# Kernel tuning notes

Hardware: AMD Instinct MI355X
Metric: run time of the kernel (lower is better)

## Reference

```python
import jax, jax.numpy as jnp
import numpy as np

T, B = 32, 64
D_IN = 512      # input_size == embedding dim
H = 512         # hidden_size
V = 32000       # n_vocab
F_FEAT = 768    # feature_size
NH = 8          # num_heads
HD = H // NH    # head_dim


def setup_inputs() -> dict:
    key = jax.random.key(0)
    ks = jax.random.split(key, 16)
    s = 0.02
    inp = {
        'y': jax.random.randint(ks[0], (T, B), 0, V),
        'ctx': jax.random.normal(ks[1], (1, B, F_FEAT), jnp.float32),
        'emb_W': jax.random.normal(ks[2], (V, D_IN), jnp.float32) * s,
        # GRUCell dec0: gates ordered (r, z, n) as in torch
        'W_ih': jax.random.normal(ks[3], (3 * H, D_IN), jnp.float32) * s,
        'b_ih': jnp.zeros((3 * H,), jnp.float32),
        'W_hh': jax.random.normal(ks[4], (3 * H, H), jnp.float32) * s,
        'b_hh': jnp.zeros((3 * H,), jnp.float32),
        # FF att: feature_size -> hidden, tanh
        'W_att': jax.random.normal(ks[5], (H, F_FEAT), jnp.float32) * s,
        'b_att': jnp.zeros((H,), jnp.float32),
        # MultiHeadSelfAttention projections (hidden -> hidden)
        'Wq': jax.random.normal(ks[6], (H, H), jnp.float32) * s,
        'bq': jnp.zeros((H,), jnp.float32),
        'Wk': jax.random.normal(ks[7], (H, H), jnp.float32) * s,
        'bk': jnp.zeros((H,), jnp.float32),
        'Wv': jax.random.normal(ks[8], (H, H), jnp.float32) * s,
        'bv': jnp.zeros((H,), jnp.float32),
        'Wfc': jax.random.normal(ks[9], (H, H), jnp.float32) * s,
        'bfc': jnp.zeros((H,), jnp.float32),
        # FF hid2out: hidden -> input, tanh, bias_zero
        'W_h2o': jax.random.normal(ks[10], (D_IN, H), jnp.float32) * s,
        'b_h2o': jnp.zeros((D_IN,), jnp.float32),
        # FF out2prob: input -> vocab, linear
        'W_out': jax.random.normal(ks[11], (V, D_IN), jnp.float32) * s,
        'b_out': jnp.zeros((V,), jnp.float32),
    }
    return inp


def reference(y, ctx, emb_W, W_ih, b_ih, W_hh, b_hh, W_att, b_att,
              Wq, bq, Wk, bk, Wv, bv, Wfc, bfc, W_h2o, b_h2o, W_out, b_out):
    y_emb = emb_W[y]                                   # [T, B, D_IN]
    # ct is constant across decode steps: tanh FF over pooled image feature
    ct = jnp.tanh(ctx[0] @ W_att.T + b_att)            # [B, H]
    h0 = jnp.zeros((y.shape[1], H), y_emb.dtype)       # dec_init 'zero'

    def step(h, y_t):
        # torch GRUCell (gate order r, z, n)
        gi = y_t @ W_ih.T + b_ih                       # [B, 3H]
        gh = h @ W_hh.T + b_hh                         # [B, 3H]
        gi_r, gi_z, gi_n = jnp.split(gi, 3, axis=-1)
        gh_r, gh_z, gh_n = jnp.split(gh, 3, axis=-1)
        r = jax.nn.sigmoid(gi_r + gh_r)
        z = jax.nn.sigmoid(gi_z + gh_z)
        n = jnp.tanh(gi_n + r * gh_n)
        h1 = (1.0 - z) * n + z * h                     # [B, H]

        x = h1 * ct                                    # [B, H]
        # MultiHeadSelfAttention on a single vector, heads act as sequence
        q = (x @ Wq.T + bq).reshape(-1, NH, HD)        # [B, NH, HD]
        k = (x @ Wk.T + bk).reshape(-1, NH, HD)
        v = (x @ Wv.T + bv).reshape(-1, NH, HD)
        scores = jnp.einsum('bhd,bgd->bhg', q, k) / HD  # note: /head_dim (not sqrt)
        attw = jax.nn.softmax(scores, axis=-1)
        att_out = jnp.einsum('bhg,bgd->bhd', attw, v).reshape(-1, H)
        h2 = att_out @ Wfc.T + bfc                     # [B, H] (fc_out, vocab_size==H)

        logit = jnp.tanh(h2 @ W_h2o.T + b_h2o)         # [B, D_IN]
        prob = jax.nn.softmax(logit @ W_out.T + b_out, axis=-1)  # [B, V]
        return h1, prob                                # f_next returns h1 as next state

    _, probs = jax.lax.scan(step, h0, y_emb)           # [T, B, V]
    return probs
```

## Files before the change

### kernel.cpp

```cpp
#include <hip/hip_runtime.h>
#include <hip/hip_bf16.h>
#include <math.h>

typedef __bf16 bf16_t;
typedef __bf16 bf16x8 __attribute__((ext_vector_type(8)));
typedef __bf16 bf16x4 __attribute__((ext_vector_type(4)));
typedef float  f32x4  __attribute__((ext_vector_type(4)));

#define T_STEPS 32
#define BATCH   64
#define DIN     512
#define HID     512
#define VOCAB   32000
#define FFEAT   768
#define ROWS    2048
#define G3      1536
#define NBLK_A  32

#define EPI_F32  0
#define EPI_BF16 1
#define EPI_TANH 2

#define GLOAD16(gp, lp) __builtin_amdgcn_global_load_lds( \
    (const __attribute__((address_space(1))) void*)(gp),  \
    (__attribute__((address_space(3))) void*)(lp), 16, 0, 0)

#define PHASEK(BUF, MH, KS, STAGE_STMT, GATE_STMT)                            \
  {                                                                           \
    bf16x8 af_[4], bf_[4];                                                    \
    _Pragma("unroll")                                                         \
    for (int m2 = 0; m2 < 4; ++m2) {                                          \
      const int row = wm * 64 + m2 * 16 + la;                                 \
      const int sl = ((KS) * 4 + lg) ^ (row & 7);                             \
      af_[m2] =                                                               \
          *(const bf16x8*)&lds[((BUF)*4 + (MH)) * 8192 + row * 64 + sl * 8];  \
    }                                                                         \
    _Pragma("unroll")                                                         \
    for (int nj = 0; nj < 4; ++nj) {                                          \
      const int row = wn * 32 + (nj & 1) * 16 + la;                           \
      const int sl = ((KS) * 4 + lg) ^ (row & 7);                             \
      bf_[nj] =                                                               \
          *(const bf16x8*)&lds[((BUF)*4 + 2 + (nj >> 1)) * 8192 + row * 64 + sl * 8];\
    }                                                                         \
    STAGE_STMT;                                                               \
    GATE_STMT;                                                                \
    __builtin_amdgcn_s_barrier();                                             \
    __builtin_amdgcn_s_setprio(1);                                            \
    _Pragma("unroll")                                                         \
    for (int m2 = 0; m2 < 4; ++m2)                                            \
      _Pragma("unroll")                                                       \
      for (int nj = 0; nj < 4; ++nj)                                          \
        acc[(MH)*4 + m2][nj] =                                                \
            __builtin_amdgcn_mfma_f32_16x16x32_bf16(                          \
                af_[m2], bf_[nj], acc[(MH)*4 + m2][nj], 0, 0, 0);             \
    __builtin_amdgcn_s_setprio(0);                                            \
    __builtin_amdgcn_s_barrier();                                             \
  }

template<int KD>
__global__ __launch_bounds__(512, 2) void gemm_v(
    const bf16_t* __restrict__ A, const bf16_t* __restrict__ B,
    const float* __restrict__ bias, bf16_t* __restrict__ ecache,
    float* __restrict__ partial, int M, int N, int NB)
{
  __shared__ bf16_t lds[2 * 4 * 8192];
  __shared__ float psum[256][4];
  const int tid = threadIdx.x;
  const int lane = tid & 63, wv = tid >> 6;
  const int wm = wv >> 2, wn = wv & 3;
  const int la = lane & 15, lg = lane >> 4;

  const int lin = blockIdx.x;
  const int mt = M >> 8;
  const int cpx = (NB * mt) >> 3;
  const int wg = (lin & 7) * cpx + (lin >> 3);
  const int bn = wg / mt, bm = wg - bn * mt;

  auto stageA = [&](int buf, int h, int kt) {
    const size_t base = (size_t)(bm * 256 + h * 128) * KD + (size_t)kt * 64;
#pragma unroll
    for (int q = 0; q < 2; ++q) {
      const int L = q * 512 + tid;
      const int row = L >> 3, sl = L & 7;
      const int c = sl ^ (row & 7);
      GLOAD16(A + base + (size_t)row * KD + c * 8,
              &lds[(buf * 4 + h) * 8192 + L * 8]);
    }
  };
  auto stageB = [&](int buf, int h, int kt) {
    const size_t base = (size_t)(bn * 256 + h * 128) * KD + (size_t)kt * 64;
#pragma unroll
    for (int q = 0; q < 2; ++q) {
      const int L = q * 512 + tid;
      const int row = L >> 3, sl = L & 7;
      const int c = sl ^ (row & 7);
      GLOAD16(B + base + (size_t)row * KD + c * 8,
              &lds[(buf * 4 + 2 + h) * 8192 + L * 8]);
    }
  };

  f32x4 acc[8][4] = {};
  constexpr int NITER = KD >> 7;

  stageA(0, 0, 0); stageA(0, 1, 0); stageB(0, 0, 0); stageB(0, 1, 0);
  stageA(1, 0, 1);
  asm volatile("s_waitcnt vmcnt(2)" ::: "memory");
  __builtin_amdgcn_s_barrier();

#pragma unroll
  for (int it = 0; it < NITER; ++it) {
    const int t0 = 2 * it;
    const bool lastI = (it == NITER - 1);
    PHASEK(0, 0, 0, { stageA(1, 1, t0 + 1); stageB(1, 0, t0 + 1); }, ;)
    PHASEK(0, 0, 1, { stageB(1, 1, t0 + 1); }, ;)
    PHASEK(0, 1, 0, { if (!lastI) stageA(0, 0, t0 + 2); }, ;)
    PHASEK(0, 1, 1, { },
           { if (lastI) { asm volatile("s_waitcnt vmcnt(0)" ::: "memory"); }
             else       { asm volatile("s_waitcnt vmcnt(2)" ::: "memory"); } })
    PHASEK(1, 0, 0, { if (!lastI) { stageA(0, 1, t0 + 2); stageB(0, 0, t0 + 2); } }, ;)
    PHASEK(1, 0, 1, { if (!lastI) stageB(0, 1, t0 + 2); }, ;)
    PHASEK(1, 1, 0, { if (!lastI) stageA(1, 0, t0 + 3); }, ;)
    PHASEK(1, 1, 1, { },
           { if (!lastI) { asm volatile("s_waitcnt vmcnt(2)" ::: "memory"); } })
  }

  float bv[4];
#pragma unroll
  for (int nj = 0; nj < 4; ++nj) {
    const int col = bn * 256 + (nj >> 1) * 128 + wn * 32 + (nj & 1) * 16 + la;
    bv[nj] = bias[col];
  }
  const int odd = la & 1;
#pragma unroll
  for (int mi = 0; mi < 8; ++mi) {
#pragma unroll
    for (int rr = 0; rr < 4; ++rr) {
      const int rowl = (mi >> 2) * 128 + wm * 64 + (mi & 3) * 16 + lg * 4 + rr;
      const int row = bm * 256 + rowl;
      float vsum = 0.f;
#pragma unroll
      for (int nj = 0; nj < 4; ++nj) {
        const float e = expf(acc[mi][nj][rr] + bv[nj]);
        vsum += e;
        const unsigned int mine =
            (unsigned int)__builtin_bit_cast(unsigned short, (bf16_t)e);
        const unsigned int other = (unsigned int)__shfl_xor((int)mine, 1);
        if (!odd) {
          const int col = bn * 256 + (nj >> 1) * 128 + wn * 32 + (nj & 1) * 16 + la;
          *(unsigned int*)&ecache[(size_t)row * N + col] = mine | (other << 16);
        }
      }
      vsum += __shfl_xor(vsum, 1);
      vsum += __shfl_xor(vsum, 2);
      vsum += __shfl_xor(vsum, 4);
      vsum += __shfl_xor(vsum, 8);
      if (la == 0) psum[rowl][wn] = vsum;
    }
  }
  __syncthreads();
  if (tid < 256) {
    partial[(size_t)(bm * 256 + tid) * NB + bn] =
        psum[tid][0] + psum[tid][1] + psum[tid][2] + psum[tid][3];
  }
}

template<int EPI, int KD>
__global__ __launch_bounds__(256) void gemm_lds(
    const bf16_t* __restrict__ A, const bf16_t* __restrict__ B,
    const float* __restrict__ bias, void* __restrict__ out, int M, int N)
{
  __shared__ bf16_t As[3][128 * 32];
  __shared__ bf16_t Bs[3][128 * 32];

  const int lane = threadIdx.x & 63;
  const int wv   = threadIdx.x >> 6;
  const int wm = wv >> 1, wn = wv & 1;
  const int bn = blockIdx.x, bm = blockIdx.y;
  const int la = lane & 15, lg = lane >> 4;
  const int tid = threadIdx.x;

  auto stage = [&](int buf, int k0) {
#pragma unroll
    for (int q = 0; q < 2; ++q) {
      const int idx = q * 256 + tid;
      const int row = idx >> 2, c = idx & 3;
      const int gch = c ^ ((row >> 1) & 3);
      GLOAD16(A + (size_t)(bm * 128 + row) * KD + k0 + gch * 8, &As[buf][idx * 8]);
      GLOAD16(B + (size_t)(bn * 128 + row) * KD + k0 + gch * 8, &Bs[buf][idx * 8]);
    }
  };
  const int rdch = (lg ^ ((la >> 1) & 3)) * 8;

  f32x4 acc[4][4] = {};
  constexpr int NT = KD >> 5;
  stage(0, 0);
  stage(1, 32);
  for (int kt = 0; kt < NT; ++kt) {
    if (kt + 1 < NT) {
      asm volatile("s_waitcnt vmcnt(4)" ::: "memory");
    } else {
      asm volatile("s_waitcnt vmcnt(0)" ::: "memory");
    }
    __builtin_amdgcn_s_barrier();
    __builtin_amdgcn_sched_barrier(0);
    if (kt + 2 < NT) stage((kt + 2) % 3, (kt + 2) * 32);
    const bf16_t* Ab = As[kt % 3];
    const bf16_t* Bb = Bs[kt % 3];
    bf16x8 a[4], b[4];
#pragma unroll
    for (int i = 0; i < 4; ++i)
      a[i] = *(const bf16x8*)(Ab + (wm * 64 + i * 16 + la) * 32 + rdch);
#pragma unroll
    for (int j = 0; j < 4; ++j)
      b[j] = *(const bf16x8*)(Bb + (wn * 64 + j * 16 + la) * 32 + rdch);
    __builtin_amdgcn_s_setprio(1);
#pragma unroll
    for (int i = 0; i < 4; ++i)
#pragma unroll
      for (int j = 0; j < 4; ++j)
        acc[i][j] = __builtin_amdgcn_mfma_f32_16x16x32_bf16(a[i], b[j], acc[i][j], 0, 0, 0);
    __builtin_amdgcn_s_setprio(0);
  }

  const int m0 = bm * 128 + wm * 64;
  const int n0 = bn * 128 + wn * 64;
  float bv4[4];
#pragma unroll
  for (int j = 0; j < 4; ++j) bv4[j] = bias[n0 + j * 16 + la];
#pragma unroll
  for (int i = 0; i < 4; ++i) {
#pragma unroll
    for (int r = 0; r < 4; ++r) {
      const int row = m0 + i * 16 + lg * 4 + r;
#pragma unroll
      for (int j = 0; j < 4; ++j) {
        const int col = n0 + j * 16 + la;
        float v = acc[i][j][r] + bv4[j];
        if constexpr (EPI == EPI_F32) {
          ((float*)out)[(size_t)row * N + col] = v;
        } else if constexpr (EPI == EPI_BF16) {
          ((bf16_t*)out)[(size_t)row * N + col] = (bf16_t)v;
        } else {
          ((bf16_t*)out)[(size_t)row * N + col] = (bf16_t)tanhf(v);
        }
      }
    }
  }
}

__global__ __launch_bounds__(256) void phaseA_k(
    const bf16_t* __restrict__ Wg, const float* __restrict__ bhh,
    const float* __restrict__ gi, const float* __restrict__ ct,
    unsigned int* __restrict__ hbuf, bf16_t* __restrict__ Xall,
    int* __restrict__ flags, const float* __restrict__ Wout_f32,
    bf16_t* __restrict__ WoutB)
{
  __shared__ bf16_t Wl[48 * 520];
  __shared__ float bl[48];
  const int tid = threadIdx.x, blk = blockIdx.x;

  if (blk >= NBLK_A) {
    const int NCB = gridDim.x - NBLK_A;
    const int n4 = VOCAB * DIN / 4;
    for (int i = (blk - NBLK_A) * 256 + tid; i < n4; i += NCB * 256) {
      float4 v = ((const float4*)Wout_f32)[i];
      bf16x4 o = {(bf16_t)v.x, (bf16_t)v.y, (bf16_t)v.z, (bf16_t)v.w};
      *(bf16x4*)(WoutB + (size_t)i * 4) = o;
    }
    return;
  }

  for (int i = tid; i < 48 * 64; i += 256) {
    const int rw = i >> 6, ch = (i & 63) << 3;
    *(bf16x8*)(Wl + rw * 520 + ch) = *(const bf16x8*)(Wg + (size_t)(blk * 48 + rw) * 512 + ch);
  }
  if (tid < 48) bl[tid] = bhh[blk * 48 + tid];
  __syncthreads();

  const int lane = tid & 63, wv = tid >> 6;
  const int la = lane & 15, lg = lane >> 4;
  const int jcol = blk * 16 + la;
  const int rowA = wv * 16 + la;

  const float blr = bl[la], blz = bl[16 + la], bln = bl[32 + la];
  float hprev[4], ctv[4];
#pragma unroll
  for (int r = 0; r < 4; ++r) {
    hprev[r] = 0.f;
    ctv[r] = ct[(size_t)(wv * 16 + lg * 4 + r) * HID + jcol];
  }

  for (int t = 0; t < T_STEPS; ++t) {
    const float* girow = gi + (size_t)t * BATCH * G3 + (size_t)blk * 48;
    float gv[12];
#pragma unroll
    for (int r = 0; r < 4; ++r) {
      const float* gp = girow + (size_t)(wv * 16 + lg * 4 + r) * G3;
      gv[r * 3 + 0] = gp[la];
      gv[r * 3 + 1] = gp[16 + la];
      gv[r * 3 + 2] = gp[32 + la];
    }
    if (t > 0) {
      if (lane < 32) {
        while (__hip_atomic_load(&flags[(lane * 4 + wv) * 16], __ATOMIC_RELAXED,
                                 __HIP_MEMORY_SCOPE_AGENT) < t) { }
      }
      asm volatile("" ::: "memory");
    }
    const unsigned long long* hb =
        (const unsigned long long*)(hbuf + (size_t)(t & 1) * 16384);
    bf16x8 af[16];
#pragma unroll
    for (int q = 0; q < 16; ++q) {
      union { unsigned long long u[2]; bf16x8 v; } c;
      const size_t bidx = (size_t)(2 * q + (lg >> 1)) * 256 + rowA * 4 + (lg & 1) * 2;
      c.u[0] = __hip_atomic_load(hb + bidx,     __ATOMIC_RELAXED, __HIP_MEMORY_SCOPE_AGENT);
      c.u[1] = __hip_atomic_load(hb + bidx + 1, __ATOMIC_RELAXED, __HIP_MEMORY_SCOPE_AGENT);
      af[q] = c.v;
    }
    f32x4 acc0 = {}, acc1 = {}, acc2 = {};
#pragma unroll
    for (int q = 0; q < 16; ++q) {
      const bf16_t* wp = Wl + q * 32 + lg * 8;
      bf16x8 b0 = *(const bf16x8*)(wp + (0 * 16 + la) * 520);
      bf16x8 b1 = *(const bf16x8*)(wp + (1 * 16 + la) * 520);
      bf16x8 b2 = *(const bf16x8*)(wp + (2 * 16 + la) * 520);
      acc0 = __builtin_amdgcn_mfma_f32_16x16x32_bf16(af[q], b0, acc0, 0, 0, 0);
      acc1 = __builtin_amdgcn_mfma_f32_16x16x32_bf16(af[q], b1, acc1, 0, 0, 0);
      acc2 = __builtin_amdgcn_mfma_f32_16x16x32_bf16(af[q], b2, acc2, 0, 0, 0);
    }
    float h1v[4];
#pragma unroll
    for (int r = 0; r < 4; ++r) {
      const float ghr = acc0[r] + blr;
      const float ghz = acc1[r] + blz;
      const float ghn = acc2[r] + bln;
      const float rr = 1.f / (1.f + expf(-(gv[r * 3 + 0] + ghr)));
      const float zz = 1.f / (1.f + expf(-(gv[r * 3 + 1] + ghz)));
      const float nn = tanhf(gv[r * 3 + 2] + rr * ghn);
      h1v[r] = (1.f - zz) * nn + zz * hprev[r];
      hprev[r] = h1v[r];
    }
    unsigned int* hn = hbuf + (size_t)((t + 1) & 1) * 16384 + blk * 512;
#pragma unroll
    for (int r = 0; r < 4; ++r) {
      const int row = wv * 16 + lg * 4 + r;
      const unsigned int mine =
          (unsigned int)__builtin_bit_cast(unsigned short, (bf16_t)h1v[r]);
      const unsigned int other = (unsigned int)__shfl_xor((int)mine, 1);
      if ((la & 1) == 0) {
        __hip_atomic_store(hn + row * 8 + (la >> 1), mine | (other << 16),
                           __ATOMIC_RELAXED, __HIP_MEMORY_SCOPE_AGENT);
      }
    }
    asm volatile("s_waitcnt vmcnt(0)" ::: "memory");
    if (lane == 0) {
      __hip_atomic_store(&flags[(blk * 4 + wv) * 16], t + 1, __ATOMIC_RELAXED,
                         __HIP_MEMORY_SCOPE_AGENT);
    }
#pragma unroll
    for (int r = 0; r < 4; ++r) {
      const int row = wv * 16 + lg * 4 + r;
      Xall[((size_t)t * BATCH + row) * HID + jcol] = (bf16_t)(h1v[r] * ctv[r]);
    }
  }
}

__global__ __launch_bounds__(256) void attn_k(const bf16_t* __restrict__ QKV,
                                              bf16_t* __restrict__ attO)
{
  __shared__ float sq[4][512], sk[4][512], sv[4][512], sw[4][64];
  const int tid = threadIdx.x;
  const int wv = tid >> 6, lane = tid & 63;
  const int row = blockIdx.x * 4 + wv;
  const bf16_t* base = QKV + (size_t)row * G3;
  bf16x8 vq = *(const bf16x8*)(base + lane * 8);
  bf16x8 vk = *(const bf16x8*)(base + 512 + lane * 8);
  bf16x8 vv = *(const bf16x8*)(base + 1024 + lane * 8);
#pragma unroll
  for (int e = 0; e < 8; ++e) {
    sq[wv][lane * 8 + e] = (float)vq[e];
    sk[wv][lane * 8 + e] = (float)vk[e];
    sv[wv][lane * 8 + e] = (float)vv[e];
  }
  __syncthreads();
  const int h = lane >> 3, g = lane & 7;
  float s = 0.f;
#pragma unroll 16
  for (int d = 0; d < 64; ++d) s += sq[wv][h * 64 + d] * sk[wv][g * 64 + d];
  s *= (1.f / 64.f);
  float m = s;
  m = fmaxf(m, __shfl_xor(m, 1));
  m = fmaxf(m, __shfl_xor(m, 2));
  m = fmaxf(m, __shfl_xor(m, 4));
  const float e = expf(s - m);
  float sum = e;
  sum += __shfl_xor(sum, 1);
  sum += __shfl_xor(sum, 2);
  sum += __shfl_xor(sum, 4);
  sw[wv][lane] = e / sum;
  __syncthreads();
#pragma unroll
  for (int rep = 0; rep < 8; ++rep) {
    const int idx = rep * 64 + lane;
    const int hh = idx >> 6, d = idx & 63;
    float o = 0.f;
#pragma unroll
    for (int gg = 0; gg < 8; ++gg) o += sw[wv][hh * 8 + gg] * sv[wv][gg * 64 + d];
    attO[(size_t)row * HID + idx] = (bf16_t)o;
  }
}

__global__ __launch_bounds__(256) void cast5_k(
    const float* __restrict__ s0, const float* __restrict__ s1,
    const float* __restrict__ s2, const float* __restrict__ s3,
    const float* __restrict__ s4, bf16_t* __restrict__ Wqkv,
    bf16_t* __restrict__ WfcB, bf16_t* __restrict__ Wh2oB)
{
  const int seg = blockIdx.x >> 8;
  const int i = (blockIdx.x & 255) * 256 + threadIdx.x;
  const float* src = seg == 0 ? s0 : seg == 1 ? s1 : seg == 2 ? s2
                   : seg == 3 ? s3 : s4;
  bf16_t* dst = seg <= 2 ? Wqkv + (size_t)seg * HID * DIN
              : seg == 3 ? WfcB : Wh2oB;
  float4 v = ((const float4*)src)[i];
  bf16x4 o = {(bf16_t)v.x, (bf16_t)v.y, (bf16_t)v.z, (bf16_t)v.w};
  *(bf16x4*)(dst + (size_t)i * 4) = o;
}

__global__ __launch_bounds__(256) void perm_cast_k(const float* __restrict__ src,
                                                   bf16_t* __restrict__ dst)
{
  const int i = blockIdx.x * 256 + threadIdx.x;
  const int pg = i >> 7, kq = (i & 127) << 2;
  const int g = pg / 48, rem = pg - g * 48, sec = rem >> 4, jj = rem & 15;
  const int srow = sec * 512 + g * 16 + jj;
  float4 v = *(const float4*)(src + (size_t)srow * DIN + kq);
  bf16x4 o = {(bf16_t)v.x, (bf16_t)v.y, (bf16_t)v.z, (bf16_t)v.w};
  *(bf16x4*)(dst + (size_t)pg * DIN + kq) = o;
}

__global__ void perm_bias_k(const float* __restrict__ bih, const float* __restrict__ bhh,
                            float* __restrict__ bihp, float* __restrict__ bhhp)
{
  const int pg = blockIdx.x * 256 + threadIdx.x;
  if (pg >= G3) return;
  const int g = pg / 48, rem = pg - g * 48, sec = rem >> 4, jj = rem & 15;
  const int srow = sec * 512 + g * 16 + jj;
  bihp[pg] = bih[srow];
  bhhp[pg] = bhh[srow];
}

__global__ void bcat_k(const float* __restrict__ a, const float* __restrict__ b,
                       const float* __restrict__ c, float* __restrict__ d)
{
  const int i = blockIdx.x * 256 + threadIdx.x;
  if (i >= G3) return;
  d[i] = i < 512 ? a[i] : (i < 1024 ? b[i - 512] : c[i - 1024]);
}

__global__ __launch_bounds__(256) void yemb_k(const int* __restrict__ y,
                                              const float* __restrict__ embW,
                                              bf16_t* __restrict__ out)
{
  const int idx = blockIdx.x * 256 + threadIdx.x;
  const int rb = idx >> 6, c = (idx & 63) << 3;
  const int tok = y[rb];
  const float4* s = (const float4*)(embW + (size_t)tok * DIN + c);
  float4 v0 = s[0], v1 = s[1];
  bf16x8 o = {(bf16_t)v0.x, (bf16_t)v0.y, (bf16_t)v0.z, (bf16_t)v0.w,
              (bf16_t)v1.x, (bf16_t)v1.y, (bf16_t)v1.z, (bf16_t)v1.w};
  *(bf16x8*)(out + (size_t)rb * DIN + c) = o;
}

__global__ __launch_bounds__(256) void ct_k(const float* __restrict__ ctx,
                                            const float* __restrict__ Watt,
                                            const float* __restrict__ batt,
                                            float* __restrict__ ct)
{
  const int idx = blockIdx.x * 256 + threadIdx.x;
  const int b = idx >> 9, j = idx & 511;
  const float4* c4 = (const float4*)(ctx + (size_t)b * FFEAT);
  const float4* w4 = (const float4*)(Watt + (size_t)j * FFEAT);
  float s = batt[j];
  for (int q = 0; q < FFEAT / 4; ++q) {
    float4 cc = c4[q], ww = w4[q];
    s += cc.x * ww.x + cc.y * ww.y + cc.z * ww.z + cc.w * ww.w;
  }
  ct[idx] = tanhf(s);
}

__global__ __launch_bounds__(256) void reduce_rows(const float* __restrict__ partial,
                                                   float* __restrict__ rowsum, int NB)
{
  const int wv = threadIdx.x >> 6, lane = threadIdx.x & 63;
  const int row = blockIdx.x * 4 + wv;
  float s = 0.f;
  for (int c = lane; c < NB; c += 64) s += partial[(size_t)row * NB + c];
  for (int m = 1; m < 64; m <<= 1) s += __shfl_xor(s, m);
  if (lane == 0) rowsum[row] = s;
}

__global__ __launch_bounds__(256) void normalize_k(const bf16_t* __restrict__ e,
                                                   const float* __restrict__ rowsum,
                                                   float* __restrict__ out)
{
  const int row = blockIdx.y;
  const int c8 = blockIdx.x * 256 + threadIdx.x;
  if (c8 >= VOCAB / 8) return;
  const float inv = 1.0f / rowsum[row];
  const size_t base = (size_t)row * VOCAB + (size_t)c8 * 8;
  bf16x8 v = *(const bf16x8*)(e + base);
  float4 o0 = {(float)v[0] * inv, (float)v[1] * inv, (float)v[2] * inv, (float)v[3] * inv};
  float4 o1 = {(float)v[4] * inv, (float)v[5] * inv, (float)v[6] * inv, (float)v[7] * inv};
  *(float4*)(out + base) = o0;
  *(float4*)(out + base + 4) = o1;
}

extern "C" void kernel_launch(void* const* d_in, const int* in_sizes, int n_in,
                              void* d_out, int out_size, void* d_ws, size_t ws_size,
                              hipStream_t stream)
{
  const int*   y     = (const int*)  d_in[0];
  const float* ctx   = (const float*)d_in[1];
  const float* embW  = (const float*)d_in[2];
  const float* W_ih  = (const float*)d_in[3];
  const float* b_ih  = (const float*)d_in[4];
  const float* W_hh  = (const float*)d_in[5];
  const float* b_hh  = (const float*)d_in[6];
  const float* W_att = (const float*)d_in[7];
  const float* b_att = (const float*)d_in[8];
  const float* Wq    = (const float*)d_in[9];
  const float* bq    = (const float*)d_in[10];
  const float* Wk    = (const float*)d_in[11];
  const float* bk    = (const float*)d_in[12];
  const float* Wv    = (const float*)d_in[13];
  const float* bv    = (const float*)d_in[14];
  const float* Wfc   = (const float*)d_in[15];
  const float* bfc   = (const float*)d_in[16];
  const float* Wh2o  = (const float*)d_in[17];
  const float* bh2o  = (const float*)d_in[18];
  const float* W_out = (const float*)d_in[19];
  const float* b_out = (const float*)d_in[20];

  char* p = (char*)d_ws;
  auto alloc = [&](size_t bytes) {
    char* r = p;
    p += (bytes + 255) & ~(size_t)255;
    return r;
  };
  bf16_t* WoutB   = (bf16_t*)alloc((size_t)VOCAB * DIN * 2);
  bf16_t* WgIh    = (bf16_t*)alloc((size_t)G3 * DIN * 2);
  bf16_t* WgHh    = (bf16_t*)alloc((size_t)G3 * DIN * 2);
  bf16_t* Wqkv    = (bf16_t*)alloc((size_t)G3 * DIN * 2);
  bf16_t* WfcB    = (bf16_t*)alloc((size_t)HID * HID * 2);
  bf16_t* Wh2oB   = (bf16_t*)alloc((size_t)HID * HID * 2);
  float*  bIhP    = (float*)alloc(G3 * 4);
  float*  bHhP    = (float*)alloc(G3 * 4);
  float*  bQkv    = (float*)alloc(G3 * 4);
  bf16_t* Yemb    = (bf16_t*)alloc((size_t)ROWS * DIN * 2);
  float*  giP     = (float*)alloc((size_t)ROWS * G3 * 4);
  float*  ctB     = (float*)alloc((size_t)BATCH * HID * 4);
  unsigned int* hbuf = (unsigned int*)alloc((size_t)2 * 16384 * 4);
  bf16_t* Xall    = (bf16_t*)alloc((size_t)ROWS * DIN * 2);
  bf16_t* QKV     = (bf16_t*)alloc((size_t)ROWS * G3 * 2);
  bf16_t* attO    = (bf16_t*)alloc((size_t)ROWS * HID * 2);
  bf16_t* h2B     = (bf16_t*)alloc((size_t)ROWS * HID * 2);
  bf16_t* logit   = (bf16_t*)alloc((size_t)ROWS * DIN * 2);
  float*  partial = (float*)alloc((size_t)ROWS * 125 * 4);
  float*  rowsum  = (float*)alloc((size_t)ROWS * 4);
  int*    flags   = (int*)alloc(32 * 4 * 64);
  bf16_t* eCache  = (bf16_t*)alloc((size_t)ROWS * VOCAB * 2);

  hipMemsetAsync(hbuf, 0, (size_t)2 * 16384 * 4, stream);
  hipMemsetAsync(flags, 0, 32 * 4 * 64, stream);

  cast5_k<<<1280, 256, 0, stream>>>(Wq, Wk, Wv, Wfc, Wh2o, Wqkv, WfcB, Wh2oB);
  perm_cast_k<<<768, 256, 0, stream>>>(W_ih, WgIh);
  perm_cast_k<<<768, 256, 0, stream>>>(W_hh, WgHh);
  perm_bias_k<<<6, 256, 0, stream>>>(b_ih, b_hh, bIhP, bHhP);
  bcat_k<<<6, 256, 0, stream>>>(bq, bk, bv, bQkv);
  yemb_k<<<512, 256, 0, stream>>>(y, embW, Yemb);
  ct_k<<<128, 256, 0, stream>>>(ctx, W_att, b_att, ctB);

  gemm_lds<EPI_F32, DIN><<<dim3(12, 16), 256, 0, stream>>>(
      Yemb, WgIh, bIhP, giP, ROWS, G3);

  phaseA_k<<<224, 256, 0, stream>>>(WgHh, bHhP, giP, ctB, hbuf, Xall, flags,
                                    W_out, WoutB);

  gemm_lds<EPI_BF16, DIN><<<dim3(12, 16), 256, 0, stream>>>(
      Xall, Wqkv, bQkv, QKV, ROWS, G3);

  attn_k<<<512, 256, 0, stream>>>(QKV, attO);

  gemm_lds<EPI_BF16, HID><<<dim3(4, 16), 256, 0, stream>>>(
      attO, WfcB, bfc, h2B, ROWS, HID);

  gemm_lds<EPI_TANH, HID><<<dim3(4, 16), 256, 0, stream>>>(
      h2B, Wh2oB, bh2o, logit, ROWS, DIN);

  gemm_v<DIN><<<1000, 512, 0, stream>>>(
      logit, WoutB, b_out, eCache, partial, ROWS, VOCAB, 125);
  reduce_rows<<<512, 256, 0, stream>>>(partial, rowsum, 125);
  normalize_k<<<dim3(16, ROWS), 256, 0, stream>>>(eCache, rowsum, (float*)d_out);
}
```

Baseline: 455.4 us.

## Fuse input-gate GEMM into recurrent kernel with flag-gated overlap; simplify vocab GEMM pipeline

The separate gi = Yemb·W_ihᵀ GEMM launch is folded into phaseA_k. Its 192 helper blocks each compute one 128x128 tile, store it with atomics and bump a per-row-block flag. The recurrent blocks spin on that flag before consuming each pair of timesteps, so the input projection overlaps the serial GRU recurrence instead of preceding it. The vocab GEMM's 8-phase macro pipeline is also replaced by a simpler per-k-tile double-buffered loop with fewer barriers. The risks are spin-wait latency, helper blocks tying up CUs that the recurrence needs, and possibly less overlap of loads with compute in the vocab GEMM.

```diff
diff --git a/kernel.cpp b/kernel.cpp
--- a/kernel.cpp
+++ b/kernel.cpp
@@ -16,6 +16,7 @@
 #define ROWS    2048
 #define G3      1536
 #define NBLK_A  32
+#define NBLK_GI 192
 
 #define EPI_F32  0
 #define EPI_BF16 1
@@ -25,7 +26,7 @@
     (const __attribute__((address_space(1))) void*)(gp),  \
     (__attribute__((address_space(3))) void*)(lp), 16, 0, 0)
 
-#define PHASEK(BUF, MH, KS, STAGE_STMT, GATE_STMT)                            \
+#define PHASEQ(BUF, MH, KS)                                                   \
   {                                                                           \
     bf16x8 af_[4], bf_[4];                                                    \
     _Pragma("unroll")                                                         \
@@ -42,9 +43,6 @@
       bf_[nj] =                                                               \
           *(const bf16x8*)&lds[((BUF)*4 + 2 + (nj >> 1)) * 8192 + row * 64 + sl * 8];\
     }                                                                         \
-    STAGE_STMT;                                                               \
-    GATE_STMT;                                                                \
-    __builtin_amdgcn_s_barrier();                                             \
     __builtin_amdgcn_s_setprio(1);                                            \
     _Pragma("unroll")                                                         \
     for (int m2 = 0; m2 < 4; ++m2)                                            \
@@ -54,7 +52,6 @@
             __builtin_amdgcn_mfma_f32_16x16x32_bf16(                          \
                 af_[m2], bf_[nj], acc[(MH)*4 + m2][nj], 0, 0, 0);             \
     __builtin_amdgcn_s_setprio(0);                                            \
-    __builtin_amdgcn_s_barrier();                                             \
   }
 
 template<int KD>
@@ -100,28 +97,33 @@
   };
 
   f32x4 acc[8][4] = {};
-  constexpr int NITER = KD >> 7;
+  constexpr int NT = KD >> 6;
 
   stageA(0, 0, 0); stageA(0, 1, 0); stageB(0, 0, 0); stageB(0, 1, 0);
-  stageA(1, 0, 1);
-  asm volatile("s_waitcnt vmcnt(2)" ::: "memory");
-  __builtin_amdgcn_s_barrier();
-
-#pragma unroll
-  for (int it = 0; it < NITER; ++it) {
-    const int t0 = 2 * it;
-    const bool lastI = (it == NITER - 1);
-    PHASEK(0, 0, 0, { stageA(1, 1, t0 + 1); stageB(1, 0, t0 + 1); }, ;)
-    PHASEK(0, 0, 1, { stageB(1, 1, t0 + 1); }, ;)
-    PHASEK(0, 1, 0, { if (!lastI) stageA(0, 0, t0 + 2); }, ;)
-    PHASEK(0, 1, 1, { },
-           { if (lastI) { asm volatile("s_waitcnt vmcnt(0)" ::: "memory"); }
-             else       { asm volatile("s_waitcnt vmcnt(2)" ::: "memory"); } })
-    PHASEK(1, 0, 0, { if (!lastI) { stageA(0, 1, t0 + 2); stageB(0, 0, t0 + 2); } }, ;)
-    PHASEK(1, 0, 1, { if (!lastI) stageB(0, 1, t0 + 2); }, ;)
-    PHASEK(1, 1, 0, { if (!lastI) stageA(1, 0, t0 + 3); }, ;)
-    PHASEK(1, 1, 1, { },
-           { if (!lastI) { asm volatile("s_waitcnt vmcnt(2)" ::: "memory"); } })
+  stageA(1, 0, 1); stageA(1, 1, 1); stageB(1, 0, 1); stageB(1, 1, 1);
+
+#pragma unroll
+  for (int kt = 0; kt < NT; ++kt) {
+    const int buf = kt & 1;
+    if (kt == 0) {
+      asm volatile("s_waitcnt vmcnt(8)" ::: "memory");
+    } else if (kt == NT - 1) {
+      asm volatile("s_waitcnt vmcnt(0)" ::: "memory");
+    } else {
+      asm volatile("s_waitcnt vmcnt(2)" ::: "memory");
+    }
+    __builtin_amdgcn_s_barrier();
+    if (kt > 0 && kt + 1 < NT) {
+      stageA(buf ^ 1, 1, kt + 1);
+      stageB(buf ^ 1, 0, kt + 1);
+      stageB(buf ^ 1, 1, kt + 1);
+    }
+    PHASEQ(buf, 0, 0)
+    PHASEQ(buf, 0, 1)
+    __builtin_amdgcn_s_barrier();
+    if (kt + 2 < NT) stageA(buf, 0, kt + 2);
+    PHASEQ(buf, 1, 0)
+    PHASEQ(buf, 1, 1)
   }
 
   float bv[4];
@@ -250,19 +252,90 @@
 
 __global__ __launch_bounds__(256) void phaseA_k(
     const bf16_t* __restrict__ Wg, const float* __restrict__ bhh,
-    const float* __restrict__ gi, const float* __restrict__ ct,
+    float* __restrict__ gi, const float* __restrict__ ct,
     unsigned int* __restrict__ hbuf, bf16_t* __restrict__ Xall,
     int* __restrict__ flags, const float* __restrict__ Wout_f32,
-    bf16_t* __restrict__ WoutB)
+    bf16_t* __restrict__ WoutB, const bf16_t* __restrict__ Yemb,
+    const bf16_t* __restrict__ WgIh, const float* __restrict__ bIhP)
 {
   __shared__ bf16_t Wl[48 * 520];
   __shared__ float bl[48];
+  __shared__ bf16_t As2[3][128 * 32];
+  __shared__ bf16_t Bs2[3][128 * 32];
   const int tid = threadIdx.x, blk = blockIdx.x;
 
   if (blk >= NBLK_A) {
-    const int NCB = gridDim.x - NBLK_A;
+    const int s = blk - NBLK_A;
+    const int bm = s / 12, bn = s - bm * 12;
+    const int lane = tid & 63, wv = tid >> 6;
+    const int wm = wv >> 1, wn = wv & 1;
+    const int la = lane & 15, lg = lane >> 4;
+
+    auto stage = [&](int buf, int k0) {
+#pragma unroll
+      for (int q = 0; q < 2; ++q) {
+        const int idx = q * 256 + tid;
+        const int row = idx >> 2, c = idx & 3;
+        const int gch = c ^ ((row >> 1) & 3);
+        GLOAD16(Yemb + (size_t)(bm * 128 + row) * DIN + k0 + gch * 8, &As2[buf][idx * 8]);
+        GLOAD16(WgIh + (size_t)(bn * 128 + row) * DIN + k0 + gch * 8, &Bs2[buf][idx * 8]);
+      }
+    };
+    const int rdch = (lg ^ ((la >> 1) & 3)) * 8;
+    f32x4 acc[4][4] = {};
+    stage(0, 0);
+    stage(1, 32);
+    for (int kt = 0; kt < 16; ++kt) {
+      if (kt + 1 < 16) { asm volatile("s_waitcnt vmcnt(4)" ::: "memory"); }
+      else             { asm volatile("s_waitcnt vmcnt(0)" ::: "memory"); }
+      __builtin_amdgcn_s_barrier();
+      __builtin_amdgcn_sched_barrier(0);
+      if (kt + 2 < 16) stage((kt + 2) % 3, (kt + 2) * 32);
+      const bf16_t* Ab = As2[kt % 3];
+      const bf16_t* Bb = Bs2[kt % 3];
+      bf16x8 a[4], b[4];
+#pragma unroll
+      for (int i = 0; i < 4; ++i)
+        a[i] = *(const bf16x8*)(Ab + (wm * 64 + i * 16 + la) * 32 + rdch);
+#pragma unroll
+      for (int j = 0; j < 4; ++j)
+        b[j] = *(const bf16x8*)(Bb + (wn * 64 + j * 16 + la) * 32 + rdch);
+      __builtin_amdgcn_s_setprio(1);
+#pragma unroll
+      for (int i = 0; i < 4; ++i)
+#pragma unroll
+        for (int j = 0; j < 4; ++j)
+          acc[i][j] = __builtin_amdgcn_mfma_f32_16x16x32_bf16(a[i], b[j], acc[i][j], 0, 0, 0);
+      __builtin_amdgcn_s_setprio(0);
+    }
+    const int m0 = bm * 128 + wm * 64;
+    const int n0 = bn * 128 + wn * 64;
+    float bv4[4];
+#pragma unroll
+    for (int j = 0; j < 4; ++j) bv4[j] = bIhP[n0 + j * 16 + la];
+#pragma unroll
+    for (int i = 0; i < 4; ++i) {
+#pragma unroll
+      for (int r = 0; r < 4; ++r) {
+        const int row = m0 + i * 16 + lg * 4 + r;
+#pragma unroll
+        for (int j = 0; j < 4; ++j) {
+          const int col = n0 + j * 16 + la;
+          const float v = acc[i][j][r] + bv4[j];
+          __hip_atomic_store((unsigned int*)&gi[(size_t)row * G3 + col],
+                             __builtin_bit_cast(unsigned int, v),
+                             __ATOMIC_RELAXED, __HIP_MEMORY_SCOPE_AGENT);
+        }
+      }
+    }
+    asm volatile("s_waitcnt vmcnt(0)" ::: "memory");
+    __syncthreads();
+    if (tid == 0) {
+      __hip_atomic_fetch_add(&flags[2048 + bm * 16], 1, __ATOMIC_RELAXED,
+                             __HIP_MEMORY_SCOPE_AGENT);
+    }
     const int n4 = VOCAB * DIN / 4;
-    for (int i = (blk - NBLK_A) * 256 + tid; i < n4; i += NCB * 256) {
+    for (int i = s * 256 + tid; i < n4; i += NBLK_GI * 256) {
       float4 v = ((const float4*)Wout_f32)[i];
       bf16x4 o = {(bf16_t)v.x, (bf16_t)v.y, (bf16_t)v.z, (bf16_t)v.w};
       *(bf16x4*)(WoutB + (size_t)i * 4) = o;
@@ -291,6 +364,11 @@
   }
 
   for (int t = 0; t < T_STEPS; ++t) {
+    if ((t & 1) == 0) {
+      while (__hip_atomic_load(&flags[2048 + (t >> 1) * 16], __ATOMIC_RELAXED,
+                               __HIP_MEMORY_SCOPE_AGENT) < 12) { }
+      asm volatile("" ::: "memory");
+    }
     const float* girow = gi + (size_t)t * BATCH * G3 + (size_t)blk * 48;
     float gv[12];
 #pragma unroll
@@ -569,11 +647,11 @@
   bf16_t* logit   = (bf16_t*)alloc((size_t)ROWS * DIN * 2);
   float*  partial = (float*)alloc((size_t)ROWS * 125 * 4);
   float*  rowsum  = (float*)alloc((size_t)ROWS * 4);
-  int*    flags   = (int*)alloc(32 * 4 * 64);
+  int*    flags   = (int*)alloc(16384);
   bf16_t* eCache  = (bf16_t*)alloc((size_t)ROWS * VOCAB * 2);
 
   hipMemsetAsync(hbuf, 0, (size_t)2 * 16384 * 4, stream);
-  hipMemsetAsync(flags, 0, 32 * 4 * 64, stream);
+  hipMemsetAsync(flags, 0, 16384, stream);
 
   cast5_k<<<1280, 256, 0, stream>>>(Wq, Wk, Wv, Wfc, Wh2o, Wqkv, WfcB, Wh2oB);
   perm_cast_k<<<768, 256, 0, stream>>>(W_ih, WgIh);
@@ -583,11 +661,8 @@
   yemb_k<<<512, 256, 0, stream>>>(y, embW, Yemb);
   ct_k<<<128, 256, 0, stream>>>(ctx, W_att, b_att, ctB);
 
-  gemm_lds<EPI_F32, DIN><<<dim3(12, 16), 256, 0, stream>>>(
-      Yemb, WgIh, bIhP, giP, ROWS, G3);
-
-  phaseA_k<<<224, 256, 0, stream>>>(WgHh, bHhP, giP, ctB, hbuf, Xall, flags,
-                                    W_out, WoutB);
+  phaseA_k<<<NBLK_A + NBLK_GI, 256, 0, stream>>>(
+      WgHh, bHhP, giP, ctB, hbuf, Xall, flags, W_out, WoutB, Yemb, WgIh, bIhP);
 
   gemm_lds<EPI_BF16, DIN><<<dim3(12, 16), 256, 0, stream>>>(
       Xall, Wqkv, bQkv, QKV, ROWS, G3);
```

Result: faster. 440.0 us (median of 5 runs) (-3.4%).
